# Kernel tuning notes

Hardware: AMD Instinct MI355X
Metric: run time of the kernel (lower is better)

## Reference

```python
import jax, jax.numpy as jnp
import numpy as np

B, T, E, H, FF = 8, 1024, 1024, 16, 4096
HD = E // H
SCALE = HD ** -0.5
EPS = 1e-12  # LayerNorm eps from TransformerLayer


def layer_norm(x, w, b):
    u = x.mean(-1, keepdims=True)
    s = ((x - u) ** 2).mean(-1, keepdims=True)  # biased variance, as in module
    return w * (x - u) / jnp.sqrt(s + EPS) + b


def setup_inputs() -> dict:
    key = jax.random.key(0)
    ks = jax.random.split(key, 8)
    std = 0.02  # nn.init.normal_(std=0.02)
    x = jax.random.normal(ks[0], (B, T, E), jnp.float32)
    # padding mask: positions >= length are padding (1 = ignore); ensure no all-masked row
    lengths = jax.random.randint(ks[1], (B,), T // 2, T + 1)
    self_padding_mask = jnp.arange(T)[None, :] >= lengths[:, None]
    # causal mask from SelfAttentionMask: triu(ones, 1)
    attn_mask = jnp.triu(jnp.ones((T, T), dtype=bool), 1)
    in_w = std * jax.random.normal(ks[2], (3 * E, E), jnp.float32)
    in_b = jnp.zeros((3 * E,), jnp.float32)
    out_w = std * jax.random.normal(ks[3], (E, E), jnp.float32)
    out_b = jnp.zeros((E,), jnp.float32)
    fc1_w = std * jax.random.normal(ks[4], (FF, E), jnp.float32)
    fc1_b = jnp.zeros((FF,), jnp.float32)
    fc2_w = std * jax.random.normal(ks[5], (E, FF), jnp.float32)
    fc2_b = jnp.zeros((E,), jnp.float32)
    ln1_w = jnp.ones((E,), jnp.float32)
    ln1_b = jnp.zeros((E,), jnp.float32)
    ln2_w = jnp.ones((E,), jnp.float32)
    ln2_b = jnp.zeros((E,), jnp.float32)
    return dict(x=x, in_w=in_w, in_b=in_b, out_w=out_w, out_b=out_b,
                fc1_w=fc1_w, fc1_b=fc1_b, fc2_w=fc2_w, fc2_b=fc2_b,
                ln1_w=ln1_w, ln1_b=ln1_b, ln2_w=ln2_w, ln2_b=ln2_b,
                self_padding_mask=self_padding_mask, attn_mask=attn_mask)


def reference(x, in_w, in_b, out_w, out_b, fc1_w, fc1_b, fc2_w, fc2_b,
              ln1_w, ln1_b, ln2_w, ln2_b, self_padding_mask, attn_mask):
    b, t, e = x.shape
    # --- self attention sublayer ---
    residual = x
    qkv = x @ in_w.T + in_b                       # [B,T,3E] fused in_proj (qkv_same path)
    q, k, v = jnp.split(qkv, 3, axis=-1)
    q = (q * SCALE).reshape(b, t, H, HD)
    k = k.reshape(b, t, H, HD)
    v = v.reshape(b, t, H, HD)
    scores = jnp.einsum('bqhd,bkhd->bhqk', q, k)  # [B,H,T,T]
    mask = attn_mask[None, None, :, :] | self_padding_mask[:, None, None, :]
    scores = jnp.where(mask, -jnp.inf, scores)
    p = jax.nn.softmax(scores, axis=-1)
    attn = jnp.einsum('bhqk,bkhd->bqhd', p, v).reshape(b, t, e)
    attn = attn @ out_w.T + out_b
    x = layer_norm(residual + attn, ln1_w, ln1_b)
    # --- feed-forward sublayer ---
    residual = x
    h = jax.nn.relu(x @ fc1_w.T + fc1_b)
    x = layer_norm(residual + (h @ fc2_w.T + fc2_b), ln2_w, ln2_b)
    return x
```

## Files before the change

kernel.cpp:

```cpp
#include <hip/hip_runtime.h>

typedef unsigned short u16;
typedef __attribute__((ext_vector_type(8))) short short8;
typedef __attribute__((ext_vector_type(4))) short short4v;
typedef __attribute__((ext_vector_type(4))) float f32x4;

#define DEV static __device__ __forceinline__

DEV float bf2f(u16 h) {
    union { unsigned int u; float f; } v; v.u = ((unsigned int)h) << 16; return v.f;
}
DEV u16 f2bf(float f) {
    union { float f; unsigned int u; } v; v.f = f;
    unsigned int r = (v.u + 0x7fff + ((v.u >> 16) & 1)) >> 16;
    return (u16)r;
}
DEV float ldx(const void* p, size_t i, int f32) {
    return f32 ? ((const float*)p)[i] : bf2f(((const u16*)p)[i]);
}

#define GLD16(g, l) __builtin_amdgcn_global_load_lds( \
    (const __attribute__((address_space(1))) void*)(g), \
    (__attribute__((address_space(3))) void*)(l), 16, 0, 0)

#define STAGE(P, pf32, eoff, dst8) do {                                        \
    if (!(pf32)) { GLD16(((const u16*)(P)) + (eoff), (dst8)); }                \
    else {                                                                     \
        const float* _p = ((const float*)(P)) + (eoff);                        \
        f32x4 _a = *(const f32x4*)_p, _b = *(const f32x4*)(_p + 4);            \
        short8 _s;                                                             \
        _s[0]=(short)f2bf(_a[0]); _s[1]=(short)f2bf(_a[1]);                    \
        _s[2]=(short)f2bf(_a[2]); _s[3]=(short)f2bf(_a[3]);                    \
        _s[4]=(short)f2bf(_b[0]); _s[5]=(short)f2bf(_b[1]);                    \
        _s[6]=(short)f2bf(_b[2]); _s[7]=(short)f2bf(_b[3]);                    \
        *(short8*)(dst8) = _s;                                                 \
    } } while (0)

__global__ __launch_bounds__(64) void probe_kernel(
    const void* __restrict__ x, const void* __restrict__ pad,
    int* __restrict__ flags, int* __restrict__ flagsA)
{
    const int lane = threadIdx.x;
    const u16* xu = (const u16*)x;
    const unsigned int e = (xu[lane * 2] >> 7) & 0xFF;
    const int sane = (e >= 0x70 && e <= 0x8F) ? 1 : 0;
    unsigned long long m = __ballot(sane);
    const int f32 = (__popcll(m) < 32) ? 1 : 0;

    const unsigned int* pi = (const unsigned int*)pad;
    int bytes = 0;
#pragma unroll
    for (int j = 0; j < 6; j++) {
        unsigned int v = pi[128 + j * 64 + lane];
        if (v > 1u) bytes = 1;
    }
    m = __ballot(bytes);
    if (lane == 0) {
        flags[0] = f32; flags[1] = (m != 0ULL) ? 1 : 0;
        flagsA[0] = 0;  flagsA[1] = 0;
    }
}

__global__ __launch_bounds__(256) void conv4(
    const void* __restrict__ src, u16* __restrict__ dst, int n4,
    const int* __restrict__ flags)
{
    const int i = blockIdx.x * 256 + threadIdx.x;
    if (i >= n4) return;
    if (flags[0]) {
        f32x4 v = ((const f32x4*)src)[i];
        short4v s;
        s[0] = (short)f2bf(v[0]); s[1] = (short)f2bf(v[1]);
        s[2] = (short)f2bf(v[2]); s[3] = (short)f2bf(v[3]);
        ((short4v*)dst)[i] = s;
    } else {
        ((short4v*)dst)[i] = ((const short4v*)src)[i];
    }
}

__global__ __launch_bounds__(256) void mask_to_bias(
    const void* __restrict__ pad, float* __restrict__ out,
    const int* __restrict__ flags)
{
    const int i = blockIdx.x * 256 + threadIdx.x;
    const int mv = flags[1] ? (int)((const unsigned char*)pad)[i]
                            : ((const int*)pad)[i];
    out[i] = mv ? -1e30f : 0.0f;
}

#define GEMM_CORE(Av, ASEL, a_row0, Wv, w_off, ldw, K)                        \
    __shared__ __align__(16) u16 As[128 * 32];                                \
    __shared__ __align__(16) u16 Bs[128 * 32];                                \
    const int inf32 = flags[0];                                               \
    const int af32  = (ASEL) ? inf32 : 0;                                     \
    const int tid  = threadIdx.x;                                             \
    const int lane = tid & 63;                                                \
    const int wave = tid >> 6;                                                \
    const int lc   = lane & 15;                                               \
    const int quad = lane >> 4;                                               \
    const int m0 = blockIdx.x * 128;                                          \
    const int n0 = blockIdx.y * 128;                                          \
    const int wm = (wave >> 1) * 64;                                          \
    const int wn = (wave & 1) * 64;                                           \
    const int r0 = tid >> 2;                                                  \
    const int ko = (tid & 3) * 8;                                             \
    f32x4 acc[4][4] = {};                                                     \
    for (int k0 = 0; k0 < (K); k0 += 32) {                                    \
        STAGE(Av, af32, ((size_t)(a_row0) + m0 + r0) * (K) + k0 + ko,         \
              &As[tid * 8]);                                                  \
        STAGE(Av, af32, ((size_t)(a_row0) + m0 + r0 + 64) * (K) + k0 + ko,    \
              &As[2048 + tid * 8]);                                           \
        STAGE(Wv, inf32, (size_t)(w_off) + (size_t)(n0 + r0) * (ldw) + k0 + ko,\
              &Bs[tid * 8]);                                                  \
        STAGE(Wv, inf32, (size_t)(w_off) + (size_t)(n0 + r0 + 64) * (ldw) + k0 + ko,\
              &Bs[2048 + tid * 8]);                                           \
        __syncthreads();                                                      \
        short8 afr[4], bfr[4];                                                \
        const int qd = quad * 8;                                              \
        _Pragma("unroll")                                                     \
        for (int mt = 0; mt < 4; mt++)                                        \
            afr[mt] = *(const short8*)&As[(wm + mt * 16 + lc) * 32 + qd];     \
        _Pragma("unroll")                                                     \
        for (int nt = 0; nt < 4; nt++)                                        \
            bfr[nt] = *(const short8*)&Bs[(wn + nt * 16 + lc) * 32 + qd];     \
        _Pragma("unroll")                                                     \
        for (int mt = 0; mt < 4; mt++)                                        \
            _Pragma("unroll")                                                 \
            for (int nt = 0; nt < 4; nt++)                                    \
                acc[mt][nt] = __builtin_amdgcn_mfma_f32_16x16x32_bf16(        \
                    afr[mt], bfr[nt], acc[mt][nt], 0, 0, 0);                  \
        __syncthreads();                                                      \
    }                                                                         \
    const int ce0 = n0 + wn + lc;                                             \
    const int re0 = m0 + wm + quad * 4;

template<int EPI>
__global__ __launch_bounds__(256, 2) void gemm_bt(
    const void* __restrict__ A, int a_sel, long a_row0,
    const void* __restrict__ W, long w_off,
    const void* __restrict__ bias, long b_off,
    const void* __restrict__ resid, int r_sel, long r_row0,
    u16* __restrict__ C, long c_row0,
    int N, int K, int ldw, const int* __restrict__ flags)
{
    GEMM_CORE(A, a_sel, a_row0, W, w_off, ldw, K)
    const int rf32 = r_sel ? inf32 : 0;
#pragma unroll
    for (int mt = 0; mt < 4; mt++) {
#pragma unroll
        for (int nt = 0; nt < 4; nt++) {
            const int c = ce0 + nt * 16;
            const float bv = ldx(bias, (size_t)b_off + c, inf32);
#pragma unroll
            for (int i = 0; i < 4; i++) {
                const int r = re0 + mt * 16 + i;
                float v = acc[mt][nt][i] + bv;
                if (EPI == 1)
                    v += ldx(resid, ((size_t)r_row0 + r) * N + c, rf32);
                if (EPI == 2) v = fmaxf(v, 0.0f);
                C[((size_t)c_row0 + r) * N + c] = f2bf(v);
            }
        }
    }
}

__global__ __launch_bounds__(256, 2) void gemm_qkv(
    const void* __restrict__ A, long a_row0,
    const void* __restrict__ W, const void* __restrict__ bias,
    u16* __restrict__ Qo, u16* __restrict__ Ko, u16* __restrict__ Vt,
    const int* __restrict__ flags)
{
    GEMM_CORE(A, 1, a_row0, W, 0, 1024, 1024)
    if (n0 < 1024) {
#pragma unroll
        for (int mt = 0; mt < 4; mt++)
#pragma unroll
            for (int nt = 0; nt < 4; nt++) {
                const int c = ce0 + nt * 16;
                const float bv = ldx(bias, c, inf32);
#pragma unroll
                for (int i = 0; i < 4; i++) {
                    const int r = re0 + mt * 16 + i;
                    Qo[((size_t)a_row0 + r) * 1024 + c] =
                        f2bf((acc[mt][nt][i] + bv) * 0.125f);
                }
            }
    } else if (n0 < 2048) {
#pragma unroll
        for (int mt = 0; mt < 4; mt++)
#pragma unroll
            for (int nt = 0; nt < 4; nt++) {
                const int c = ce0 + nt * 16;
                const float bv = ldx(bias, c, inf32);
#pragma unroll
                for (int i = 0; i < 4; i++) {
                    const int r = re0 + mt * 16 + i;
                    Ko[(size_t)r * 1024 + (c - 1024)] = f2bf(acc[mt][nt][i] + bv);
                }
            }
    } else {
#pragma unroll
        for (int mt = 0; mt < 4; mt++)
#pragma unroll
            for (int nt = 0; nt < 4; nt++) {
                const int c = ce0 + nt * 16;
                const float bv = ldx(bias, c, inf32);
                const int cv = c - 2048;
                const int hh = cv >> 6, d = cv & 63;
                const int rb = re0 + mt * 16;
                const int bl = rb >> 10, t = rb & 1023;
                short4v pk;
#pragma unroll
                for (int i = 0; i < 4; i++)
                    pk[i] = (short)f2bf(acc[mt][nt][i] + bv);
                *(short4v*)&Vt[((size_t)(bl * 16 + hh) * 64 + d) * 1024 + t] = pk;
            }
    }
}

__global__ __launch_bounds__(256, 2) void gemm_accf32(
    const void* __restrict__ A, const void* __restrict__ W, long w_off,
    const void* __restrict__ bias, const u16* __restrict__ resid, long r_row0,
    float* __restrict__ C, int ldw, int init, const int* __restrict__ flags)
{
    GEMM_CORE(A, 0, 0, W, w_off, ldw, 1024)
#pragma unroll
    for (int mt = 0; mt < 4; mt++) {
#pragma unroll
        for (int nt = 0; nt < 4; nt++) {
            const int c = ce0 + nt * 16;
            const float bv = ldx(bias, c, inf32);
#pragma unroll
            for (int i = 0; i < 4; i++) {
                const int r = re0 + mt * 16 + i;
                float v = acc[mt][nt][i];
                if (init) v += bv + bf2f(resid[((size_t)r_row0 + r) * 1024 + c]);
                else      v += C[(size_t)r * 1024 + c];
                C[(size_t)r * 1024 + c] = v;
            }
        }
    }
}

#define GEMM8_PRE(Ag_, Wg_, Kg_)                                              \
    __shared__ __align__(16) u16 Ab[3][128 * 64];                             \
    __shared__ __align__(16) u16 Bb[3][256 * 64];                             \
    const u16* Ag = (Ag_); const u16* Wg = (Wg_); const int Kg = (Kg_);       \
    const int tid  = threadIdx.x;                                             \
    const int lane = tid & 63;                                                \
    const int lc   = lane & 15;                                               \
    const int quad = lane >> 4;                                               \
    const int w    = tid >> 6;                                                \
    const int wr   = w >> 2;                                                  \
    const int wc   = w & 3;                                                   \
    const int m0 = blockIdx.x * 128;                                          \
    const int n0 = blockIdx.y * 256;                                          \
    const int srow = tid >> 3;                                                \
    const int scol = (((tid & 7) ^ (srow & 7)) << 3);                         \
    const int sw0 = (((quad) ^ (lc & 7)) << 3);                               \
    const int sw1 = sw0 ^ 32;                                                 \
    f32x4 acc[4][4] = {};                                                     \
    short8 af[4], bf[4];

#define SA8(buf, kk) do {                                                     \
    GLD16(Ag + (size_t)(m0 + srow) * Kg + (kk) + scol, &Ab[buf][tid * 8]);    \
    GLD16(Ag + (size_t)(m0 + 64 + srow) * Kg + (kk) + scol,                   \
          &Ab[buf][4096 + tid * 8]); } while (0)
#define SB8a(buf, kk) do {                                                    \
    GLD16(Wg + (size_t)(n0 + srow) * Kg + (kk) + scol, &Bb[buf][tid * 8]);    \
    GLD16(Wg + (size_t)(n0 + 64 + srow) * Kg + (kk) + scol,                   \
          &Bb[buf][4096 + tid * 8]); } while (0)
#define SB8b(buf, kk) do {                                                    \
    GLD16(Wg + (size_t)(n0 + 128 + srow) * Kg + (kk) + scol,                  \
          &Bb[buf][8192 + tid * 8]);                                          \
    GLD16(Wg + (size_t)(n0 + 192 + srow) * Kg + (kk) + scol,                  \
          &Bb[buf][12288 + tid * 8]); } while (0)
#define LDFR(rbuf, SW) do { _Pragma("unroll")                                 \
    for (int q_ = 0; q_ < 4; q_++) {                                          \
        af[q_] = *(const short8*)&Ab[rbuf][(wr * 64 + q_ * 16 + lc) * 64 + (SW)];\
        bf[q_] = *(const short8*)&Bb[rbuf][(wc * 64 + q_ * 16 + lc) * 64 + (SW)];\
    } } while (0)
#define MFMA16 do { _Pragma("unroll")                                         \
    for (int mq = 0; mq < 4; mq++) { _Pragma("unroll")                        \
    for (int nq = 0; nq < 4; nq++)                                            \
        acc[mq][nq] = __builtin_amdgcn_mfma_f32_16x16x32_bf16(                \
            af[mq], bf[nq], acc[mq][nq], 0, 0, 0); } } while (0)

#define GEMM8_LOOP                                                            \
    const int NT = Kg >> 6;                                                   \
    SA8(0, 0); SB8a(0, 0); SB8b(0, 0);                                        \
    if (NT > 1) { SA8(1, 64); SB8a(1, 64); SB8b(1, 64); }                     \
    if (NT > 1) asm volatile("s_waitcnt vmcnt(6)" ::: "memory");              \
    else        asm volatile("s_waitcnt vmcnt(0)" ::: "memory");              \
    __builtin_amdgcn_s_barrier();                                             \
    int rb_ = 0, wb_ = 2;                                                     \
    for (int t = 0; t < NT; ++t) {                                            \
        const bool s_ = (t + 2 < NT);                                         \
        const int k2_ = (t + 2) << 6;                                         \
        LDFR(rb_, sw0);                                                       \
        if (s_) { SA8(wb_, k2_); SB8a(wb_, k2_); }                            \
        __builtin_amdgcn_s_barrier();                                         \
        asm volatile("s_waitcnt lgkmcnt(0)" ::: "memory");                    \
        __builtin_amdgcn_s_setprio(1);                                        \
        MFMA16;                                                               \
        __builtin_amdgcn_s_setprio(0);                                        \
        __builtin_amdgcn_s_barrier();                                         \
        LDFR(rb_, sw1);                                                       \
        if (s_) SB8b(wb_, k2_);                                               \
        __builtin_amdgcn_s_barrier();                                         \
        asm volatile("s_waitcnt lgkmcnt(0)" ::: "memory");                    \
        __builtin_amdgcn_s_setprio(1);                                        \
        MFMA16;                                                               \
        __builtin_amdgcn_s_setprio(0);                                        \
        if (s_) asm volatile("s_waitcnt vmcnt(6)" ::: "memory");              \
        else    asm volatile("s_waitcnt vmcnt(0)" ::: "memory");              \
        __builtin_amdgcn_s_barrier();                                         \
        rb_ = (rb_ == 2) ? 0 : rb_ + 1;                                       \
        wb_ = (wb_ == 2) ? 0 : wb_ + 1;                                       \
    }                                                                         \
    const int cb0 = n0 + wc * 64 + lc;                                        \
    const int rb0 = m0 + wr * 64 + quad * 4;

template<int EPI>
__global__ __launch_bounds__(512, 2) void gemm8(
    const u16* __restrict__ A, const u16* __restrict__ W,
    const u16* __restrict__ bias, const u16* __restrict__ resid,
    u16* __restrict__ C, int N, int K)
{
    GEMM8_PRE(A, W, K)
    GEMM8_LOOP
#pragma unroll
    for (int mq = 0; mq < 4; mq++) {
#pragma unroll
        for (int nq = 0; nq < 4; nq++) {
            const int cN = cb0 + nq * 16;
            const float bv = bf2f(bias[cN]);
#pragma unroll
            for (int i = 0; i < 4; i++) {
                const int rM = rb0 + mq * 16 + i;
                float v = acc[mq][nq][i] + bv;
                if (EPI == 1) v += bf2f(resid[(size_t)rM * N + cN]);
                if (EPI == 2) v = fmaxf(v, 0.0f);
                C[(size_t)rM * N + cN] = f2bf(v);
            }
        }
    }
}

__global__ __launch_bounds__(512, 2) void gemm8_qkv(
    const u16* __restrict__ A, const u16* __restrict__ W,
    const u16* __restrict__ bias,
    u16* __restrict__ Qo, u16* __restrict__ Ko, u16* __restrict__ Vt)
{
    GEMM8_PRE(A, W, 1024)
    GEMM8_LOOP
    if (n0 < 1024) {
#pragma unroll
        for (int mq = 0; mq < 4; mq++)
#pragma unroll
            for (int nq = 0; nq < 4; nq++) {
                const int c = cb0 + nq * 16;
                const float bv = bf2f(bias[c]);
#pragma unroll
                for (int i = 0; i < 4; i++) {
                    const int r = rb0 + mq * 16 + i;
                    Qo[(size_t)r * 1024 + c] =
                        f2bf((acc[mq][nq][i] + bv) * 0.125f);
                }
            }
    } else if (n0 < 2048) {
#pragma unroll
        for (int mq = 0; mq < 4; mq++)
#pragma unroll
            for (int nq = 0; nq < 4; nq++) {
                const int c = cb0 + nq * 16;
                const float bv = bf2f(bias[c]);
#pragma unroll
                for (int i = 0; i < 4; i++) {
                    const int r = rb0 + mq * 16 + i;
                    Ko[(size_t)r * 1024 + (c - 1024)] =
                        f2bf(acc[mq][nq][i] + bv);
                }
            }
    } else {
#pragma unroll
        for (int mq = 0; mq < 4; mq++)
#pragma unroll
            for (int nq = 0; nq < 4; nq++) {
                const int c = cb0 + nq * 16;
                const float bv = bf2f(bias[c]);
                const int cv = c - 2048;
                const int hh = cv >> 6, d = cv & 63;
                const int rbase = rb0 + mq * 16;
                const int bl = rbase >> 10, tt = rbase & 1023;
                short4v pk;
#pragma unroll
                for (int i = 0; i < 4; i++)
                    pk[i] = (short)f2bf(acc[mq][nq][i] + bv);
                *(short4v*)&Vt[((size_t)(bl * 16 + hh) * 64 + d) * 1024 + tt] = pk;
            }
    }
}

__global__ __launch_bounds__(256, 2) void attn_kernel(
    u16* __restrict__ QO, const u16* __restrict__ Ko,
    const u16* __restrict__ Vt, const float* __restrict__ kb, int b0)
{
    __shared__ __align__(16) u16 Qs[2 * 128 * 32];
    __shared__ __align__(16) u16 Ks[2][2 * 64 * 32];
    __shared__ __align__(16) u16 Vs[2][2 * 64 * 32];
    __shared__ __align__(16) u16 Ps[4][32 * 72];
    __shared__ float kba[1024];

    const int tid  = threadIdx.x;
    const int lane = tid & 63;
    const int w    = tid >> 6;
    const int lc   = lane & 15;
    const int quad = lane >> 4;
    const int bl = blockIdx.y >> 4;
    const int h  = blockIdx.y & 15;
    const int b  = b0 + bl;

    *(f32x4*)&kba[tid * 4] = *(const f32x4*)&kb[b * 1024 + tid * 4];

    for (int p = 0; p < 2; p++) {
        const int qt = p ? 7 - (int)blockIdx.x : (int)blockIdx.x;

#pragma unroll
        for (int it = 0; it < 4; it++) {
            const int kcd = it >> 1, half = it & 1;
            const int r = half * 64 + (tid >> 2);
            const int c = kcd * 32 + (tid & 3) * 8;
            GLD16(&QO[((size_t)(b * 1024 + qt * 128 + r)) * 1024 + h * 64 + c],
                  &Qs[kcd * 4096 + half * 2048 + tid * 8]);
        }
        {
            const int rr = tid >> 2;
#pragma unroll
            for (int it = 0; it < 2; it++) {
                const int cc = it * 32 + (tid & 3) * 8;
                GLD16(&Ko[((size_t)(bl * 1024 + rr)) * 1024 + h * 64 + cc],
                      &Ks[0][it * 2048 + tid * 8]);
                GLD16(&Vt[((size_t)(bl * 16 + h) * 64 + rr) * 1024 + cc],
                      &Vs[0][it * 2048 + tid * 8]);
            }
        }
        __syncthreads();

        short8 aq[2][2];
#pragma unroll
        for (int mt = 0; mt < 2; mt++)
#pragma unroll
            for (int kc = 0; kc < 2; kc++)
                aq[mt][kc] = *(const short8*)
                    &Qs[kc * 4096 + (w * 32 + mt * 16 + lc) * 32 + quad * 8];

        f32x4 o[2][4] = {};
        float m_i[2][4], l_i[2][4];
#pragma unroll
        for (int mt = 0; mt < 2; mt++)
#pragma unroll
            for (int i = 0; i < 4; i++) { m_i[mt][i] = -1e30f; l_i[mt][i] = 0.0f; }

        const int ktmax = 2 * qt + 2;
        for (int kt = 0; kt < ktmax; kt++) {
            const int cur = kt & 1;
            if (kt + 1 < ktmax) {
                const int nxt = cur ^ 1;
                const int rr = tid >> 2;
#pragma unroll
                for (int it = 0; it < 2; it++) {
                    const int cc = it * 32 + (tid & 3) * 8;
                    GLD16(&Ko[((size_t)(bl * 1024 + (kt + 1) * 64 + rr)) * 1024 + h * 64 + cc],
                          &Ks[nxt][it * 2048 + tid * 8]);
                    GLD16(&Vt[((size_t)(bl * 16 + h) * 64 + rr) * 1024 + (kt + 1) * 64 + cc],
                          &Vs[nxt][it * 2048 + tid * 8]);
                }
            }

            short8 bk[4][2];
#pragma unroll
            for (int nt = 0; nt < 4; nt++)
#pragma unroll
                for (int kc = 0; kc < 2; kc++)
                    bk[nt][kc] = *(const short8*)
                        &Ks[cur][kc * 2048 + (nt * 16 + lc) * 32 + quad * 8];

            f32x4 s[2][4];
#pragma unroll
            for (int mt = 0; mt < 2; mt++)
#pragma unroll
                for (int nt = 0; nt < 4; nt++) {
                    f32x4 z = {};
#pragma unroll
                    for (int kc = 0; kc < 2; kc++)
                        z = __builtin_amdgcn_mfma_f32_16x16x32_bf16(
                            aq[mt][kc], bk[nt][kc], z, 0, 0, 0);
                    s[mt][nt] = z;
                }

            const int causal = (kt >= 2 * qt);
            float al[2][4];
#pragma unroll
            for (int mt = 0; mt < 2; mt++) {
                const int qg0 = qt * 128 + w * 32 + mt * 16 + quad * 4;
#pragma unroll
                for (int nt = 0; nt < 4; nt++) {
                    const int kg = kt * 64 + nt * 16 + lc;
                    const float kbv = kba[kt * 64 + nt * 16 + lc];
#pragma unroll
                    for (int i = 0; i < 4; i++) {
                        float sv = s[mt][nt][i] + kbv;
                        if (causal && kg > qg0 + i) sv = -1e30f;
                        s[mt][nt][i] = sv;
                    }
                }
                float mnew[4], rs[4];
#pragma unroll
                for (int i = 0; i < 4; i++) {
                    float rm = fmaxf(fmaxf(s[mt][0][i], s[mt][1][i]),
                                     fmaxf(s[mt][2][i], s[mt][3][i]));
                    rm = fmaxf(rm, __shfl_xor(rm, 1));
                    rm = fmaxf(rm, __shfl_xor(rm, 2));
                    rm = fmaxf(rm, __shfl_xor(rm, 4));
                    rm = fmaxf(rm, __shfl_xor(rm, 8));
                    mnew[i] = fmaxf(m_i[mt][i], rm);
                    al[mt][i] = exp2f((m_i[mt][i] - mnew[i]) * 1.442695041f);
                    rs[i] = 0.0f;
                }
#pragma unroll
                for (int nt = 0; nt < 4; nt++)
#pragma unroll
                    for (int i = 0; i < 4; i++) {
                        float pp = exp2f((s[mt][nt][i] - mnew[i]) * 1.442695041f);
                        s[mt][nt][i] = pp;
                        rs[i] += pp;
                    }
#pragma unroll
                for (int i = 0; i < 4; i++) {
                    float r = rs[i];
                    r += __shfl_xor(r, 1);
                    r += __shfl_xor(r, 2);
                    r += __shfl_xor(r, 4);
                    r += __shfl_xor(r, 8);
                    l_i[mt][i] = l_i[mt][i] * al[mt][i] + r;
                    m_i[mt][i] = mnew[i];
                }
#pragma unroll
                for (int nt = 0; nt < 4; nt++)
#pragma unroll
                    for (int i = 0; i < 4; i++)
                        Ps[w][(mt * 16 + quad * 4 + i) * 72 + nt * 16 + lc] =
                            f2bf(s[mt][nt][i]);
            }

            short8 ap[2][2], bv2[4][2];
#pragma unroll
            for (int mt = 0; mt < 2; mt++)
#pragma unroll
                for (int kc = 0; kc < 2; kc++)
                    ap[mt][kc] = *(const short8*)
                        &Ps[w][(mt * 16 + lc) * 72 + kc * 32 + quad * 8];
#pragma unroll
            for (int nt = 0; nt < 4; nt++)
#pragma unroll
                for (int kc = 0; kc < 2; kc++)
                    bv2[nt][kc] = *(const short8*)
                        &Vs[cur][kc * 2048 + (nt * 16 + lc) * 32 + quad * 8];
#pragma unroll
            for (int mt = 0; mt < 2; mt++)
#pragma unroll
                for (int nt = 0; nt < 4; nt++) {
                    f32x4 oo = o[mt][nt];
#pragma unroll
                    for (int i = 0; i < 4; i++) oo[i] *= al[mt][i];
#pragma unroll
                    for (int kc = 0; kc < 2; kc++)
                        oo = __builtin_amdgcn_mfma_f32_16x16x32_bf16(
                            ap[mt][kc], bv2[nt][kc], oo, 0, 0, 0);
                    o[mt][nt] = oo;
                }
            __syncthreads();
        }

#pragma unroll
        for (int mt = 0; mt < 2; mt++)
#pragma unroll
            for (int i = 0; i < 4; i++) {
                const float inv = l_i[mt][i] > 0.0f ? 1.0f / l_i[mt][i] : 0.0f;
#pragma unroll
                for (int nt = 0; nt < 4; nt++) {
                    const int r = qt * 128 + w * 32 + mt * 16 + quad * 4 + i;
                    const int d = nt * 16 + lc;
                    QO[((size_t)(b * 1024 + r)) * 1024 + h * 64 + d] =
                        f2bf(o[mt][nt][i] * inv);
                }
            }
    }
}

template<int IN16, int OUTSEL>
__global__ __launch_bounds__(256) void ln_kernel(
    const void* __restrict__ yv, const void* __restrict__ w,
    const void* __restrict__ bb, void* __restrict__ o, long o_row0,
    const int* __restrict__ flags)
{
    const int row = blockIdx.x;
    const int tid = threadIdx.x;
    const int inf32 = flags[0];
    float x0, x1, x2, x3;
    if (IN16) {
        const u16* p = (const u16*)yv + (size_t)row * 1024 + tid * 4;
        short4v v = *(const short4v*)p;
        x0 = bf2f((u16)v[0]); x1 = bf2f((u16)v[1]);
        x2 = bf2f((u16)v[2]); x3 = bf2f((u16)v[3]);
    } else {
        const float* p = (const float*)yv + (size_t)row * 1024 + tid * 4;
        f32x4 v = *(const f32x4*)p;
        x0 = v[0]; x1 = v[1]; x2 = v[2]; x3 = v[3];
    }
    float s = x0 + x1 + x2 + x3;
    float q = x0 * x0 + x1 * x1 + x2 * x2 + x3 * x3;
#pragma unroll
    for (int off = 32; off; off >>= 1) {
        s += __shfl_xor(s, off);
        q += __shfl_xor(q, off);
    }
    __shared__ float sm[8];
    const int lane = tid & 63, wv = tid >> 6;
    if (lane == 0) { sm[wv] = s; sm[4 + wv] = q; }
    __syncthreads();
    const float ts = sm[0] + sm[1] + sm[2] + sm[3];
    const float tq = sm[4] + sm[5] + sm[6] + sm[7];
    const float mean = ts * (1.0f / 1024.0f);
    float var = tq * (1.0f / 1024.0f) - mean * mean;
    if (var < 0.0f) var = 0.0f;
    const float rinv = rsqrtf(var + 1e-12f);

    const size_t obase = ((size_t)o_row0 + row) * 1024 + tid * 4;
#pragma unroll
    for (int j = 0; j < 4; j++) {
        const int c = tid * 4 + j;
        float xv = (j == 0) ? x0 : (j == 1) ? x1 : (j == 2) ? x2 : x3;
        float v = ldx(w, c, inf32) * ((xv - mean) * rinv) + ldx(bb, c, inf32);
        if (OUTSEL && inf32) ((float*)o)[obase + j] = v;
        else                 ((u16*)o)[obase + j] = f2bf(v);
    }
}

extern "C" void kernel_launch(void* const* d_in, const int* in_sizes, int n_in,
                              void* d_out, int out_size, void* d_ws, size_t ws_size,
                              hipStream_t stream)
{
    const void* x     = d_in[0];
    const void* in_w  = d_in[1];
    const void* in_b  = d_in[2];
    const void* out_w = d_in[3];
    const void* out_b = d_in[4];
    const void* fc1_w = d_in[5];
    const void* fc1_b = d_in[6];
    const void* fc2_w = d_in[7];
    const void* fc2_b = d_in[8];
    const void* ln1w  = d_in[9];
    const void* ln1b  = d_in[10];
    const void* ln2w  = d_in[11];
    const void* ln2b  = d_in[12];
    const void* pad   = d_in[13];
    u16* outp = (u16*)d_out;
    char* ws = (char*)d_ws;
    dim3 blk(256);
    dim3 blk8(512);

    const size_t MB = 1024 * 1024;
    const bool bigWS = ws_size >= (105 * MB + 64 * 1024);

    if (bigWS) {
        u16*   xb   = (u16*)(ws + 0);
        u16*   x1   = (u16*)(ws + 0);
        u16*   w1b  = (u16*)(ws + 16 * MB);
        u16*   wob  = (u16*)(ws + 22 * MB);
        u16*   f1b  = (u16*)(ws + 24 * MB);
        u16*   f2b  = (u16*)(ws + 32 * MB);
        u16*   inbb = (u16*)(ws + 40 * MB);
        u16*   outbb= (u16*)(ws + 40 * MB + 8192);
        u16*   f1bb = (u16*)(ws + 40 * MB + 16384);
        u16*   f2bb = (u16*)(ws + 40 * MB + 24576);
        u16*   Ko   = (u16*)(ws + 41 * MB);
        u16*   Vt   = (u16*)(ws + 57 * MB);
        u16*   y1   = (u16*)(ws + 73 * MB);
        u16*   h    = (u16*)(ws + 41 * MB);
        u16*   y2   = (u16*)(ws + 16 * MB);
        int*   flags  = (int*)(ws + 105 * MB);
        int*   flagsA = (int*)(ws + 105 * MB + 32);
        float* kbias  = (float*)(ws + 105 * MB + 64);

        probe_kernel<<<dim3(1), dim3(64), 0, stream>>>(x, pad, flags, flagsA);
        mask_to_bias<<<dim3(32), blk, 0, stream>>>(pad, kbias, flags);
        conv4<<<dim3(8192), blk, 0, stream>>>(x, xb, 2097152, flags);
        conv4<<<dim3(3072), blk, 0, stream>>>(in_w, w1b, 786432, flags);
        conv4<<<dim3(1024), blk, 0, stream>>>(out_w, wob, 262144, flags);
        conv4<<<dim3(4096), blk, 0, stream>>>(fc1_w, f1b, 1048576, flags);
        conv4<<<dim3(4096), blk, 0, stream>>>(fc2_w, f2b, 1048576, flags);
        conv4<<<dim3(3), blk, 0, stream>>>(in_b, inbb, 768, flags);
        conv4<<<dim3(1), blk, 0, stream>>>(out_b, outbb, 256, flags);
        conv4<<<dim3(4), blk, 0, stream>>>(fc1_b, f1bb, 1024, flags);
        conv4<<<dim3(1), blk, 0, stream>>>(fc2_b, f2bb, 256, flags);

        gemm8_qkv<<<dim3(64, 12), blk8, 0, stream>>>(
            xb, w1b, inbb, outp, Ko, Vt);
        attn_kernel<<<dim3(4, 128), blk, 0, stream>>>(outp, Ko, Vt, kbias, 0);
        gemm8<1><<<dim3(64, 4), blk8, 0, stream>>>(
            outp, wob, outbb, xb, y1, 1024, 1024);
        ln_kernel<1, 0><<<dim3(8192), blk, 0, stream>>>(y1, ln1w, ln1b, x1, 0, flags);
        gemm8<2><<<dim3(64, 16), blk8, 0, stream>>>(
            x1, f1b, f1bb, nullptr, h, 4096, 1024);
        gemm8<1><<<dim3(64, 4), blk8, 0, stream>>>(
            h, f2b, f2bb, x1, y2, 1024, 4096);
        ln_kernel<1, 1><<<dim3(8192), blk, 0, stream>>>(y2, ln2w, ln2b, d_out, 0, flags);
    } else {
        u16*   Ko    = (u16*)(ws + 0);
        u16*   Vt    = (u16*)(ws + 4 * MB);
        u16*   y1h   = (u16*)(ws + 0);
        float* acc   = (float*)(ws + 0);
        u16*   hc    = (u16*)(ws + 8 * MB);
        int*   flags  = (int*)(ws + 12 * MB);
        int*   flagsA = (int*)(ws + 12 * MB + 32);
        float* kbias  = (float*)(ws + 12 * MB + 64);

        probe_kernel<<<dim3(1), dim3(64), 0, stream>>>(x, pad, flags, flagsA);
        mask_to_bias<<<dim3(32), blk, 0, stream>>>(pad, kbias, flags);

        for (int q = 0; q < 4; q++) {
            const long r0 = (long)q * 2048;
            gemm_qkv<<<dim3(16, 24), blk, 0, stream>>>(
                x, r0, in_w, in_b, outp, Ko, Vt, flags);
            attn_kernel<<<dim3(4, 32), blk, 0, stream>>>(
                outp, Ko, Vt, kbias, q * 2);
        }
        for (int hf = 0; hf < 2; hf++) {
            const long r0 = (long)hf * 4096;
            gemm_bt<1><<<dim3(32, 8), blk, 0, stream>>>(
                outp, 0, r0, out_w, 0, out_b, 0, x, 1, r0,
                y1h, 0, 1024, 1024, 1024, flags);
            ln_kernel<1, 0><<<dim3(4096), blk, 0, stream>>>(
                y1h, ln1w, ln1b, outp, r0, flags);
        }
        for (int q = 3; q >= 0; q--) {
            const long r0 = (long)q * 2048;
            for (int c = 0; c < 4; c++) {
                gemm_bt<2><<<dim3(16, 8), blk, 0, stream>>>(
                    outp, 0, r0, fc1_w, (long)c * 1024 * 1024, fc1_b, (long)c * 1024,
                    nullptr, 0, 0, hc, 0, 1024, 1024, 1024, flags);
                gemm_accf32<<<dim3(16, 8), blk, 0, stream>>>(
                    hc, fc2_w, (long)c * 1024, fc2_b, outp, r0,
                    acc, 4096, c == 0, flags);
            }
            ln_kernel<0, 1><<<dim3(2048), blk, 0, stream>>>(
                acc, ln2w, ln2b, d_out, r0, flags);
        }
    }
}
```

Before: 531.7 us.

## Add 256x256-tile GEMM kernel for QKV and FC1 projections

Introduces a new GEMM variant with 256x256 output tiles per 512-thread block, where each wave computes a 128x64 sub-tile split into two M halves that share B fragments. The QKV and FC1 GEMMs switch to it with half as many row blocks. The aim is to raise arithmetic intensity and cut global/LDS traffic per FLOP. The cost is more accumulator registers (128 floats per lane), which under the 2-blocks launch bound may cause spills or lower occupancy, and fewer blocks for load balance across CUs.

```diff
diff --git a/kernel.cpp b/kernel.cpp
--- a/kernel.cpp
+++ b/kernel.cpp
@@ -315,8 +315,8 @@
         if (s_) asm volatile("s_waitcnt vmcnt(6)" ::: "memory");              \
         else    asm volatile("s_waitcnt vmcnt(0)" ::: "memory");              \
         __builtin_amdgcn_s_barrier();                                         \
-        rb_ = (rb_ == 2) ? 0 : rb_ + 1;                                       \
-        wb_ = (wb_ == 2) ? 0 : wb_ + 1;                                       \
+        rb_ = (rb_ == 2) ? 0 : rb_ + 1;                                      \
+        wb_ = (wb_ == 2) ? 0 : wb_ + 1;                                      \
     }                                                                         \
     const int cb0 = n0 + wc * 64 + lc;                                        \
     const int rb0 = m0 + wr * 64 + quad * 4;
@@ -347,16 +347,120 @@
     }
 }
 
-__global__ __launch_bounds__(512, 2) void gemm8_qkv(
+#define GEMM256_PRE(Ag_, Wg_, Kg_)                                            \
+    __shared__ __align__(16) u16 Ab[3][8192];                                 \
+    __shared__ __align__(16) u16 Bb[3][8192];                                 \
+    const u16* Ag = (Ag_); const u16* Wg = (Wg_); const int Kg = (Kg_);       \
+    const int tid  = threadIdx.x;                                             \
+    const int lane = tid & 63;                                                \
+    const int lc   = lane & 15;                                               \
+    const int quad = lane >> 4;                                               \
+    const int w    = tid >> 6;                                                \
+    const int wr   = w >> 2;                                                  \
+    const int wc   = w & 3;                                                   \
+    const int m0 = blockIdx.x * 256;                                          \
+    const int n0 = blockIdx.y * 256;                                          \
+    const int s_r = tid >> 2;                                                 \
+    const int s_c = (((tid & 3) ^ ((tid >> 3) & 3)) << 3);                    \
+    const int fsw = ((quad ^ ((lc >> 1) & 3)) << 3);                          \
+    const int arow = wr * 128 + lc;                                           \
+    const int brow = wc * 64 + lc;                                            \
+    f32x4 acc[8][4] = {};                                                     \
+    short8 af[4], bf[4];
+
+#define SA256(buf, kk) do {                                                   \
+    GLD16(Ag + (size_t)(m0 + s_r) * Kg + (kk) + s_c, &Ab[buf][tid * 8]);      \
+    GLD16(Ag + (size_t)(m0 + 128 + s_r) * Kg + (kk) + s_c,                    \
+          &Ab[buf][4096 + tid * 8]); } while (0)
+#define SB256(buf, kk) do {                                                   \
+    GLD16(Wg + (size_t)(n0 + s_r) * Kg + (kk) + s_c, &Bb[buf][tid * 8]);      \
+    GLD16(Wg + (size_t)(n0 + 128 + s_r) * Kg + (kk) + s_c,                    \
+          &Bb[buf][4096 + tid * 8]); } while (0)
+#define LDA256(MH) do { _Pragma("unroll")                                     \
+    for (int q_ = 0; q_ < 4; q_++)                                            \
+        af[q_] = *(const short8*)                                             \
+            &Ab[rb_][(arow + ((MH) * 4 + q_) * 16) * 32 + fsw]; } while (0)
+#define LDB256 do { _Pragma("unroll")                                         \
+    for (int q_ = 0; q_ < 4; q_++)                                            \
+        bf[q_] = *(const short8*)                                             \
+            &Bb[rb_][(brow + q_ * 16) * 32 + fsw]; } while (0)
+#define MF256(MH) do { _Pragma("unroll")                                      \
+    for (int mq = 0; mq < 4; mq++) { _Pragma("unroll")                        \
+    for (int nq = 0; nq < 4; nq++)                                            \
+        acc[(MH) * 4 + mq][nq] = __builtin_amdgcn_mfma_f32_16x16x32_bf16(     \
+            af[mq], bf[nq], acc[(MH) * 4 + mq][nq], 0, 0, 0); } } while (0)
+
+#define GEMM256_LOOP                                                          \
+    const int NT = Kg >> 5;                                                   \
+    SA256(0, 0); SB256(0, 0);                                                 \
+    if (NT > 1) { SA256(1, 32); SB256(1, 32); }                               \
+    if (NT > 1) asm volatile("s_waitcnt vmcnt(4)" ::: "memory");              \
+    else        asm volatile("s_waitcnt vmcnt(0)" ::: "memory");              \
+    __builtin_amdgcn_s_barrier();                                             \
+    int rb_ = 0, wb_ = 2;                                                     \
+    for (int t = 0; t < NT; ++t) {                                            \
+        const bool s_ = (t + 2 < NT);                                         \
+        const int k2_ = (t + 2) << 5;                                         \
+        LDB256; LDA256(0);                                                    \
+        if (s_) SA256(wb_, k2_);                                              \
+        __builtin_amdgcn_s_barrier();                                         \
+        asm volatile("s_waitcnt lgkmcnt(0)" ::: "memory");                    \
+        __builtin_amdgcn_s_setprio(1);                                        \
+        MF256(0);                                                             \
+        __builtin_amdgcn_s_setprio(0);                                        \
+        __builtin_amdgcn_s_barrier();                                         \
+        LDA256(1);                                                            \
+        if (s_) SB256(wb_, k2_);                                              \
+        __builtin_amdgcn_s_barrier();                                         \
+        asm volatile("s_waitcnt lgkmcnt(0)" ::: "memory");                    \
+        __builtin_amdgcn_s_setprio(1);                                        \
+        MF256(1);                                                             \
+        __builtin_amdgcn_s_setprio(0);                                        \
+        if (s_) asm volatile("s_waitcnt vmcnt(4)" ::: "memory");              \
+        else    asm volatile("s_waitcnt vmcnt(0)" ::: "memory");              \
+        __builtin_amdgcn_s_barrier();                                         \
+        rb_ = (rb_ == 2) ? 0 : rb_ + 1;                                      \
+        wb_ = (wb_ == 2) ? 0 : wb_ + 1;                                      \
+    }                                                                         \
+    const int cb0 = n0 + wc * 64 + lc;                                        \
+    const int rb0 = m0 + wr * 128 + quad * 4;
+
+template<int EPI>
+__global__ __launch_bounds__(512, 2) void gemm256(
+    const u16* __restrict__ A, const u16* __restrict__ W,
+    const u16* __restrict__ bias, const u16* __restrict__ resid,
+    u16* __restrict__ C, int N, int K)
+{
+    GEMM256_PRE(A, W, K)
+    GEMM256_LOOP
+#pragma unroll
+    for (int mq = 0; mq < 8; mq++) {
+#pragma unroll
+        for (int nq = 0; nq < 4; nq++) {
+            const int cN = cb0 + nq * 16;
+            const float bv = bf2f(bias[cN]);
+#pragma unroll
+            for (int i = 0; i < 4; i++) {
+                const int rM = rb0 + mq * 16 + i;
+                float v = acc[mq][nq][i] + bv;
+                if (EPI == 1) v += bf2f(resid[(size_t)rM * N + cN]);
+                if (EPI == 2) v = fmaxf(v, 0.0f);
+                C[(size_t)rM * N + cN] = f2bf(v);
+            }
+        }
+    }
+}
+
+__global__ __launch_bounds__(512, 2) void gemm256_qkv(
     const u16* __restrict__ A, const u16* __restrict__ W,
     const u16* __restrict__ bias,
     u16* __restrict__ Qo, u16* __restrict__ Ko, u16* __restrict__ Vt)
 {
-    GEMM8_PRE(A, W, 1024)
-    GEMM8_LOOP
+    GEMM256_PRE(A, W, 1024)
+    GEMM256_LOOP
     if (n0 < 1024) {
 #pragma unroll
-        for (int mq = 0; mq < 4; mq++)
+        for (int mq = 0; mq < 8; mq++)
 #pragma unroll
             for (int nq = 0; nq < 4; nq++) {
                 const int c = cb0 + nq * 16;
@@ -370,7 +474,7 @@
             }
     } else if (n0 < 2048) {
 #pragma unroll
-        for (int mq = 0; mq < 4; mq++)
+        for (int mq = 0; mq < 8; mq++)
 #pragma unroll
             for (int nq = 0; nq < 4; nq++) {
                 const int c = cb0 + nq * 16;
@@ -384,7 +488,7 @@
             }
     } else {
 #pragma unroll
-        for (int mq = 0; mq < 4; mq++)
+        for (int mq = 0; mq < 8; mq++)
 #pragma unroll
             for (int nq = 0; nq < 4; nq++) {
                 const int c = cb0 + nq * 16;
@@ -706,13 +810,13 @@
         conv4<<<dim3(4), blk, 0, stream>>>(fc1_b, f1bb, 1024, flags);
         conv4<<<dim3(1), blk, 0, stream>>>(fc2_b, f2bb, 256, flags);
 
-        gemm8_qkv<<<dim3(64, 12), blk8, 0, stream>>>(
+        gemm256_qkv<<<dim3(32, 12), blk8, 0, stream>>>(
             xb, w1b, inbb, outp, Ko, Vt);
         attn_kernel<<<dim3(4, 128), blk, 0, stream>>>(outp, Ko, Vt, kbias, 0);
         gemm8<1><<<dim3(64, 4), blk8, 0, stream>>>(
             outp, wob, outbb, xb, y1, 1024, 1024);
         ln_kernel<1, 0><<<dim3(8192), blk, 0, stream>>>(y1, ln1w, ln1b, x1, 0, flags);
-        gemm8<2><<<dim3(64, 16), blk8, 0, stream>>>(
+        gemm256<2><<<dim3(32, 16), blk8, 0, stream>>>(
             x1, f1b, f1bb, nullptr, h, 4096, 1024);
         gemm8<1><<<dim3(64, 4), blk8, 0, stream>>>(
             h, f2b, f2bb, x1, y2, 1024, 4096);
```

New measurement: 524.2 us. About the same (-1.4%).
